# Kernel optimization log

Hardware: AMD Instinct MI355X
Metric: run time of the kernel (lower is better)

Reference implementation:

```python
import jax, jax.numpy as jnp
import numpy as np


def _lstm_dir(x, mask, W, U, b, reverse):
    """Keras-style masked LSTM over one direction.
    x: [B,T,Din], mask: [B,T] bool. Returns (ys [B,T,D], h [B,D], c [B,D]).
    Masked steps: state carried through, emitted output = previous emitted output.
    """
    B, T, _ = x.shape
    D = U.shape[0]
    # Precompute input projections for all timesteps in one big GEMM: [B,T,4D]
    xz = jnp.einsum('btd,dg->btg', x, W) + b
    xz_t = jnp.swapaxes(xz, 0, 1)            # [T,B,4D]
    m_t = jnp.swapaxes(mask, 0, 1)[..., None]  # [T,B,1]
    h0 = jnp.zeros((B, D), x.dtype)

    def step(carry, inp):
        h, c, out_prev = carry
        z_in, m = inp
        z = z_in + h @ U                      # [B,4D]
        i = jax.nn.sigmoid(z[:, :D])
        f = jax.nn.sigmoid(z[:, D:2 * D])
        g = jnp.tanh(z[:, 2 * D:3 * D])
        o = jax.nn.sigmoid(z[:, 3 * D:])
        c_new = f * c + i * g
        h_new = o * jnp.tanh(c_new)
        h = jnp.where(m, h_new, h)
        c = jnp.where(m, c_new, c)
        out = jnp.where(m, h_new, out_prev)
        return (h, c, out), out

    (h, c, _), ys = jax.lax.scan(step, (h0, h0, h0), (xz_t, m_t), reverse=reverse)
    return jnp.swapaxes(ys, 0, 1), h, c


def _bilstm(x, mask, Wf, Uf, bf, Wb, Ub, bb):
    yf, hf, cf = _lstm_dir(x, mask, Wf, Uf, bf, reverse=False)
    yb, hb, cb = _lstm_dir(x, mask, Wb, Ub, bb, reverse=True)
    return jnp.concatenate([yf, yb], axis=-1), hf, cf, hb, cb


def setup_inputs() -> dict:
    key = jax.random.key(0)
    ks = jax.random.split(key, 13)
    B, T, D = 64, 256, 512
    X = jax.random.normal(ks[0], (B, T, D), jnp.float32)
    # variable-length padding: odd batch rows valid for 3T/4 steps, zeros after
    lengths = jnp.where(jnp.arange(B) % 2 == 0, T, 3 * T // 4)
    valid = jnp.arange(T)[None, :] < lengths[:, None]
    X = X * valid[..., None].astype(jnp.float32)
    s = 0.05
    p = lambda k, shp: jax.random.normal(k, shp, jnp.float32) * s
    return {
        'X': X,
        'Wf1': p(ks[1], (D, 4 * D)), 'Uf1': p(ks[2], (D, 4 * D)), 'bf1': jnp.zeros((4 * D,), jnp.float32),
        'Wb1': p(ks[3], (D, 4 * D)), 'Ub1': p(ks[4], (D, 4 * D)), 'bb1': jnp.zeros((4 * D,), jnp.float32),
        'Wf2': p(ks[5], (2 * D, 4 * D)), 'Uf2': p(ks[6], (D, 4 * D)), 'bf2': jnp.zeros((4 * D,), jnp.float32),
        'Wb2': p(ks[7], (2 * D, 4 * D)), 'Ub2': p(ks[8], (D, 4 * D)), 'bb2': jnp.zeros((4 * D,), jnp.float32),
    }


def reference(X, Wf1, Uf1, bf1, Wb1, Ub1, bb1, Wf2, Uf2, bf2, Wb2, Ub2, bb2):
    mask = jnp.any(X != 0, axis=-1)  # Masking(mask_value=0): all-zero timesteps masked
    y1, _, _, _, _ = _bilstm(X, mask, Wf1, Uf1, bf1, Wb1, Ub1, bb1)
    H, h_fw, c_fw, h_bw, c_bw = _bilstm(y1, mask, Wf2, Uf2, bf2, Wb2, Ub2, bb2)
    hidden_state = jnp.concatenate([h_fw, h_bw], axis=-1)
    cell_state = jnp.concatenate([c_fw, c_bw], axis=-1)
    return H, hidden_state, cell_state
```

## Files before the change

### kernel.cpp

```cpp
#include <hip/hip_runtime.h>

typedef unsigned short u16;
typedef unsigned int u32;
typedef unsigned long long u64;
typedef __attribute__((ext_vector_type(8))) short bf16x8;
typedef __attribute__((ext_vector_type(4))) float f32x4;
typedef __attribute__((ext_vector_type(4))) _Float16 f16x4;

#define MFMA16(a, b, c) __builtin_amdgcn_mfma_f32_16x16x32_bf16((a), (b), (c), 0, 0, 0)

__device__ __forceinline__ u16 f2bf(float f) {
    union { float f; u32 u; } v; v.f = f;
    u32 r = v.u + 0x7FFFu + ((v.u >> 16) & 1u);
    return (u16)(r >> 16);
}
__device__ __forceinline__ float sigmoidf_(float x) {
    return 1.0f / (1.0f + __expf(-x));
}
__device__ __forceinline__ float tanhf_(float x) {
    float e = __expf(-2.0f * x);
    return (1.0f - e) / (1.0f + e);
}

__global__ void mask_cast_kernel(const float* __restrict__ X, int* __restrict__ mask,
                                 u16* __restrict__ out) {
    int row = blockIdx.x;
    int lane = threadIdx.x;
    const float* r = X + (size_t)row * 512 + lane * 8;
    float4 v0 = *(const float4*)r;
    float4 v1 = *(const float4*)(r + 4);
    int nz = (v0.x != 0.f) | (v0.y != 0.f) | (v0.z != 0.f) | (v0.w != 0.f) |
             (v1.x != 0.f) | (v1.y != 0.f) | (v1.z != 0.f) | (v1.w != 0.f);
    nz = __any(nz);
    uint4 pk;
    pk.x = (u32)f2bf(v0.x) | ((u32)f2bf(v0.y) << 16);
    pk.y = (u32)f2bf(v0.z) | ((u32)f2bf(v0.w) << 16);
    pk.z = (u32)f2bf(v1.x) | ((u32)f2bf(v1.y) << 16);
    pk.w = (u32)f2bf(v1.z) | ((u32)f2bf(v1.w) << 16);
    *(uint4*)(out + (size_t)row * 512 + lane * 8) = pk;
    if (lane == 0) mask[row] = nz ? 1 : 0;
}

struct TBatch { const float* s[6]; u16* d[6]; };
__global__ void transpose_cast_batch_kernel(TBatch tb, int K, int N) {
    const float* __restrict__ in = tb.s[blockIdx.z];
    u16* __restrict__ out = tb.d[blockIdx.z];
    __shared__ float tile[32][33];
    int k0 = blockIdx.y * 32, n0 = blockIdx.x * 32;
    int tx = threadIdx.x, ty = threadIdx.y;
    #pragma unroll
    for (int i = ty; i < 32; i += 8)
        tile[i][tx] = in[(size_t)(k0 + i) * N + (n0 + tx)];
    __syncthreads();
    #pragma unroll
    for (int i = ty; i < 32; i += 8)
        out[(size_t)(n0 + i) * K + (k0 + tx)] = f2bf(tile[tx][i]);
}

__global__ __launch_bounds__(256) void gemm_xz2_kernel(
        const u16* __restrict__ A,
        const u16* __restrict__ Btf, const u16* __restrict__ Btb,
        const float* __restrict__ biasf, const float* __restrict__ biasb,
        _Float16* __restrict__ Cf, _Float16* __restrict__ Cb, int K) {
    int w = threadIdx.x >> 6, lane = threadIdx.x & 63;
    int q = lane >> 4, col = lane & 15;
    int m0 = blockIdx.x * 256 + w * 64;
    int dir = blockIdx.y >> 4;
    int sl = blockIdx.y & 15;
    const u16* Bt = dir ? Btb : Btf;
    const float* bias = dir ? biasb : biasf;
    _Float16* C = dir ? Cb : Cf;

    const u16* arow = A + (size_t)(m0 + col) * K + q * 8;
    const u16* brow = Bt + (size_t)(sl * 32 + col) * K + q * 8;

    f32x4 acc[4][8];
    #pragma unroll
    for (int mf = 0; mf < 4; ++mf)
        #pragma unroll
        for (int j = 0; j < 8; ++j) acc[mf][j] = (f32x4){0.f, 0.f, 0.f, 0.f};

    #pragma unroll 1
    for (int kc = 0; kc < K; kc += 32) {
        bf16x8 b[8], a[4];
        #pragma unroll
        for (int j = 0; j < 8; ++j) {
            int g = j & 3, half = j >> 2;
            b[j] = *(const bf16x8*)(brow + (size_t)(g * 512 + half * 16) * K + kc);
        }
        #pragma unroll
        for (int mf = 0; mf < 4; ++mf)
            a[mf] = *(const bf16x8*)(arow + (size_t)mf * 16 * K + kc);
        #pragma unroll
        for (int mf = 0; mf < 4; ++mf)
            #pragma unroll
            for (int j = 0; j < 8; ++j)
                acc[mf][j] = MFMA16(a[mf], b[j], acc[mf][j]);
    }

    float bs[8];
    #pragma unroll
    for (int j = 0; j < 8; ++j) {
        int g = j & 3, half = j >> 2;
        bs[j] = bias[g * 512 + sl * 32 + half * 16 + col];
    }

    #pragma unroll
    for (int mf = 0; mf < 4; ++mf) {
        #pragma unroll
        for (int r = 0; r < 4; ++r) {
            int row = m0 + mf * 16 + q * 4 + r;
            int b = row >> 8, t = row & 255;
            #pragma unroll
            for (int half = 0; half < 2; ++half) {
                union { _Float16 h[4]; u64 u; } pk;
                #pragma unroll
                for (int g = 0; g < 4; ++g)
                    pk.h[g] = (_Float16)(acc[mf][half * 4 + g][r] + bs[half * 4 + g]);
                size_t uidx = (((size_t)t * 32 + (sl * 2 + half)) * 64 + b) * 16 + col;
                ((u64*)C)[uidx] = pk.u;
            }
        }
    }
}

__global__ void init_rec_kernel(u32* __restrict__ p, int n) {
    int i = blockIdx.x * 256 + threadIdx.x;
    if (i < n) p[i] = 0;
}

__global__ __launch_bounds__(256) void lstm_rec14_kernel(
        const _Float16* __restrict__ xz_f, const _Float16* __restrict__ xz_b,
        const u16* __restrict__ Ut_f, const u16* __restrict__ Ut_b,
        const int* __restrict__ mask,
        u32* __restrict__ flags,
        u16* __restrict__ hg,
        u16* __restrict__ y_bf,
        float* __restrict__ y_f32,
        float* __restrict__ hc_out)
{
    const int T = 256;
    int slice = blockIdx.x, dir = blockIdx.y;
    int tid = threadIdx.x;
    int lane = tid & 63, q = lane >> 4, col = lane & 15;
    int wv = tid >> 6;
    int ds = slice * 16, m0 = wv * 16;

    const _Float16* xz = dir ? xz_b : xz_f;
    const u16* Ut = dir ? Ut_b : Ut_f;
    u32* planeflags = flags + (dir * 128 + wv * 32) * 16;
    u32* myflag = planeflags + slice * 16;

    alignas(16) __shared__ u16 Ulds[4 * 16 * 64 * 8];
    for (int cell = tid; cell < 4096; cell += 256) {
        int l = cell & 63, fr = cell >> 6;
        int kc = fr & 15, g = fr >> 4;
        *(uint4*)&Ulds[cell * 8] =
            *(const uint4*)(Ut + (size_t)(g * 512 + ds + (l & 15)) * 512 + kc * 32 + (l >> 4) * 8);
    }

    int myrow = m0 + col;
    int cbase = myrow * 4 + (q & 1) * 2 + (q >> 1) * 256;
    int odd = col & 1;
    int r0 = q * 4 + (odd ? 2 : 0);
    size_t pbase = ((size_t)slice * 64 + m0 + r0) * 16 + (col & ~1);

    float creg[4] = {0.f, 0.f, 0.f, 0.f};
    float hreg[4] = {0.f, 0.f, 0.f, 0.f};
    __syncthreads();

    for (int it = 0; it < T; ++it) {
        int t = dir ? (T - 1 - it) : it;
        const u64* hq = (const u64*)(hg + (it & 1) * 65536 + dir * 32768);
        u16* hdst = hg + ((it & 1) ^ 1) * 65536 + dir * 32768;

        f16x4 xzv[4];
        {
            const _Float16* xzt = xz + (((size_t)t * 32 + slice) * 64) * 64;
            #pragma unroll
            for (int r = 0; r < 4; ++r)
                xzv[r] = *(const f16x4*)(xzt + ((m0 + q * 4 + r) * 16 + col) * 4);
        }
        int mk[4];
        #pragma unroll
        for (int r = 0; r < 4; ++r) mk[r] = mask[(m0 + q * 4 + r) * T + t];

        bf16x8 afr[16];
        if (it == 0) {
            #pragma unroll
            for (int c = 0; c < 16; ++c)
                afr[c] = (bf16x8){0, 0, 0, 0, 0, 0, 0, 0};
        } else {
            u32 tgt = (u32)it;
            for (;;) {
                u32 f = __hip_atomic_load(planeflags + (lane & 31) * 16,
                                          __ATOMIC_RELAXED, __HIP_MEMORY_SCOPE_AGENT);
                if (__all(f >= tgt)) break;
                __builtin_amdgcn_s_sleep(1);
            }
            __builtin_amdgcn_sched_barrier(0);
            #pragma unroll
            for (int c = 0; c < 16; ++c) {
                union { u64 qw[2]; bf16x8 v; } u;
                u.qw[0] = __hip_atomic_load(hq + c * 512 + cbase, __ATOMIC_RELAXED,
                                            __HIP_MEMORY_SCOPE_AGENT);
                u.qw[1] = __hip_atomic_load(hq + c * 512 + cbase + 1, __ATOMIC_RELAXED,
                                            __HIP_MEMORY_SCOPE_AGENT);
                afr[c] = u.v;
            }
        }

        f32x4 acc[4];
        #pragma unroll
        for (int g = 0; g < 4; ++g) acc[g] = (f32x4){0.f, 0.f, 0.f, 0.f};
        #pragma unroll
        for (int kc = 0; kc < 16; ++kc) {
            #pragma unroll
            for (int g = 0; g < 4; ++g) {
                bf16x8 b = *(const bf16x8*)&Ulds[((g * 16 + kc) * 64 + lane) * 8];
                acc[g] = MFMA16(afr[kc], b, acc[g]);
            }
        }

        u32 hbv[4];
        #pragma unroll
        for (int r = 0; r < 4; ++r) {
            float zi = acc[0][r] + (float)xzv[r][0];
            float zf = acc[1][r] + (float)xzv[r][1];
            float zg = acc[2][r] + (float)xzv[r][2];
            float zo = acc[3][r] + (float)xzv[r][3];
            float ig = sigmoidf_(zi);
            float fg = sigmoidf_(zf);
            float gg = tanhf_(zg);
            float og = sigmoidf_(zo);
            float cn = fg * creg[r] + ig * gg;
            float hn = og * tanhf_(cn);
            if (mk[r]) { creg[r] = cn; hreg[r] = hn; }
            hbv[r] = (u32)f2bf(hreg[r]);
        }

        if (it < T - 1) {
            u32 part[4];
            #pragma unroll
            for (int r = 0; r < 4; ++r) part[r] = (u32)__shfl_xor((int)hbv[r], 1);
            u32 p0 = odd ? (part[2] | (hbv[2] << 16)) : (hbv[0] | (part[0] << 16));
            u32 p1 = odd ? (part[3] | (hbv[3] << 16)) : (hbv[1] | (part[1] << 16));
            u32* w0 = (u32*)(hdst + pbase);
            u32* w1 = w0 + 8;
            __hip_atomic_store(w0, p0, __ATOMIC_RELAXED, __HIP_MEMORY_SCOPE_AGENT);
            __hip_atomic_store(w1, p1, __ATOMIC_RELAXED, __HIP_MEMORY_SCOPE_AGENT);
            asm volatile("s_waitcnt vmcnt(0)" ::: "memory");
            if (lane == 0)
                __hip_atomic_store(myflag, (u32)(it + 1), __ATOMIC_RELAXED,
                                   __HIP_MEMORY_SCOPE_AGENT);
        }

        #pragma unroll
        for (int r = 0; r < 4; ++r) {
            int b = m0 + q * 4 + r;
            size_t ybase = ((size_t)b * T + t) * 1024 + dir * 512 + ds + col;
            if (y_bf) __builtin_nontemporal_store((u16)hbv[r], y_bf + ybase);
            else      __builtin_nontemporal_store(hreg[r], y_f32 + ybase);
        }
    }

    if (hc_out) {
        #pragma unroll
        for (int r = 0; r < 4; ++r) {
            int b = m0 + q * 4 + r;
            hc_out[(size_t)b * 1024 + dir * 512 + ds + col] = hreg[r];
            hc_out[65536 + (size_t)b * 1024 + dir * 512 + ds + col] = creg[r];
        }
    }
}

extern "C" void kernel_launch(void* const* d_in, const int* in_sizes, int n_in,
                              void* d_out, int out_size, void* d_ws, size_t ws_size,
                              hipStream_t stream) {
    const float* X   = (const float*)d_in[0];
    const float* Wf1 = (const float*)d_in[1];
    const float* Uf1 = (const float*)d_in[2];
    const float* bf1 = (const float*)d_in[3];
    const float* Wb1 = (const float*)d_in[4];
    const float* Ub1 = (const float*)d_in[5];
    const float* bb1 = (const float*)d_in[6];
    const float* Wf2 = (const float*)d_in[7];
    const float* Uf2 = (const float*)d_in[8];
    const float* bf2 = (const float*)d_in[9];
    const float* Wb2 = (const float*)d_in[10];
    const float* Ub2 = (const float*)d_in[11];
    const float* bb2 = (const float*)d_in[12];
    float* out = (float*)d_out;

    u16* y1bf = (u16*)d_out;
    u16* Xbf  = (u16*)((char*)d_out + 33554432);

    char* ws = (char*)d_ws;
    size_t off = 0;
    auto alloc = [&](size_t bytes) { char* p = ws + off; off = (off + bytes + 255) & ~(size_t)255; return p; };
    u16*  Wt1f  = (u16*)alloc(2048ull * 512 * 2);
    u16*  Wt1b  = (u16*)alloc(2048ull * 512 * 2);
    u16*  Wt2f  = (u16*)alloc(2048ull * 1024 * 2);
    u16*  Wt2b  = (u16*)alloc(2048ull * 1024 * 2);
    u16*  Ut1f  = (u16*)alloc(2048ull * 512 * 2);
    u16*  Ut1b  = (u16*)alloc(2048ull * 512 * 2);
    u16*  Ut2f  = (u16*)alloc(2048ull * 512 * 2);
    u16*  Ut2b  = (u16*)alloc(2048ull * 512 * 2);
    int*  maskb = (int*)alloc(16384ull * 4);
    u32*  flags = (u32*)alloc(16384);
    u16*  hg    = (u16*)alloc(2ull * 2 * 32 * 64 * 16 * 2);
    _Float16* xzf = (_Float16*)alloc(16384ull * 2048 * 2);
    _Float16* xzb = (_Float16*)alloc(16384ull * 2048 * 2);
    (void)ws_size; (void)in_sizes; (void)n_in; (void)out_size;
    const int initN = 4096;

    mask_cast_kernel<<<dim3(16384), dim3(64), 0, stream>>>(X, maskb, Xbf);
    TBatch tb6;
    tb6.s[0] = Wf1; tb6.d[0] = Wt1f;
    tb6.s[1] = Wb1; tb6.d[1] = Wt1b;
    tb6.s[2] = Uf1; tb6.d[2] = Ut1f;
    tb6.s[3] = Ub1; tb6.d[3] = Ut1b;
    tb6.s[4] = Uf2; tb6.d[4] = Ut2f;
    tb6.s[5] = Ub2; tb6.d[5] = Ut2b;
    transpose_cast_batch_kernel<<<dim3(64, 16, 6), dim3(32, 8), 0, stream>>>(tb6, 512, 2048);
    TBatch tb2;
    tb2.s[0] = Wf2; tb2.d[0] = Wt2f;
    tb2.s[1] = Wb2; tb2.d[1] = Wt2b;
    tb2.s[2] = nullptr; tb2.d[2] = nullptr;
    tb2.s[3] = nullptr; tb2.d[3] = nullptr;
    tb2.s[4] = nullptr; tb2.d[4] = nullptr;
    tb2.s[5] = nullptr; tb2.d[5] = nullptr;
    transpose_cast_batch_kernel<<<dim3(64, 32, 2), dim3(32, 8), 0, stream>>>(tb2, 1024, 2048);

    gemm_xz2_kernel<<<dim3(64, 32), dim3(256), 0, stream>>>(
        Xbf, Wt1f, Wt1b, bf1, bb1, xzf, xzb, 512);
    init_rec_kernel<<<dim3(16), dim3(256), 0, stream>>>(flags, initN);
    lstm_rec14_kernel<<<dim3(32, 2), dim3(256), 0, stream>>>(
        xzf, xzb, Ut1f, Ut1b, maskb, flags, hg, y1bf, nullptr, nullptr);

    gemm_xz2_kernel<<<dim3(64, 32), dim3(256), 0, stream>>>(
        y1bf, Wt2f, Wt2b, bf2, bb2, xzf, xzb, 1024);
    init_rec_kernel<<<dim3(16), dim3(256), 0, stream>>>(flags, initN);
    lstm_rec14_kernel<<<dim3(32, 2), dim3(256), 0, stream>>>(
        xzf, xzb, Ut2f, Ut2b, maskb, flags, hg, nullptr, out, out + 16777216);
}
```

Before: 2.868 ms.

## Tag hidden-state words with step counter to drop store-wait fence

Hidden-state exchange now packs each 32-bit bf16 pair with the step number in the upper half of a 64-bit atomic store. Readers re-poll the data until every tag matches, so the writer no longer waits on vmcnt(0) before raising its flag. This targets the latency of the per-step cross-block handshake. In exchange the h buffer doubles in size, readers issue twice as many loads, and the init kernel must zero the larger region. The old flag poll is still done before the data poll.

```diff
diff --git a/kernel.cpp b/kernel.cpp
--- a/kernel.cpp
+++ b/kernel.cpp
@@ -129,12 +129,12 @@
     if (i < n) p[i] = 0;
 }
 
-__global__ __launch_bounds__(256) void lstm_rec14_kernel(
+__global__ __launch_bounds__(256) void lstm_rec15_kernel(
         const _Float16* __restrict__ xz_f, const _Float16* __restrict__ xz_b,
         const u16* __restrict__ Ut_f, const u16* __restrict__ Ut_b,
         const int* __restrict__ mask,
         u32* __restrict__ flags,
-        u16* __restrict__ hg,
+        u64* __restrict__ hg,
         u16* __restrict__ y_bf,
         float* __restrict__ y_f32,
         float* __restrict__ hc_out)
@@ -160,10 +160,10 @@
     }
 
     int myrow = m0 + col;
-    int cbase = myrow * 4 + (q & 1) * 2 + (q >> 1) * 256;
+    int cbase = (q >> 1) * 512 + myrow * 8 + (q & 1) * 4;
     int odd = col & 1;
     int r0 = q * 4 + (odd ? 2 : 0);
-    size_t pbase = ((size_t)slice * 64 + m0 + r0) * 16 + (col & ~1);
+    size_t pbase = ((size_t)slice * 64 + m0 + r0) * 8 + (col >> 1);
 
     float creg[4] = {0.f, 0.f, 0.f, 0.f};
     float hreg[4] = {0.f, 0.f, 0.f, 0.f};
@@ -171,8 +171,8 @@
 
     for (int it = 0; it < T; ++it) {
         int t = dir ? (T - 1 - it) : it;
-        const u64* hq = (const u64*)(hg + (it & 1) * 65536 + dir * 32768);
-        u16* hdst = hg + ((it & 1) ^ 1) * 65536 + dir * 32768;
+        const u64* hq = hg + (it & 1) * 32768 + dir * 16384;
+        u64* hdst = hg + ((it & 1) ^ 1) * 32768 + dir * 16384;
 
         f16x4 xzv[4];
         {
@@ -199,14 +199,33 @@
                 __builtin_amdgcn_s_sleep(1);
             }
             __builtin_amdgcn_sched_barrier(0);
-            #pragma unroll
-            for (int c = 0; c < 16; ++c) {
-                union { u64 qw[2]; bf16x8 v; } u;
-                u.qw[0] = __hip_atomic_load(hq + c * 512 + cbase, __ATOMIC_RELAXED,
-                                            __HIP_MEMORY_SCOPE_AGENT);
-                u.qw[1] = __hip_atomic_load(hq + c * 512 + cbase + 1, __ATOMIC_RELAXED,
-                                            __HIP_MEMORY_SCOPE_AGENT);
-                afr[c] = u.v;
+            for (;;) {
+                u64 qv[64];
+                #pragma unroll
+                for (int kc = 0; kc < 16; ++kc) {
+                    #pragma unroll
+                    for (int j = 0; j < 4; ++j)
+                        qv[kc * 4 + j] = __hip_atomic_load(hq + kc * 1024 + cbase + j,
+                                                           __ATOMIC_RELAXED,
+                                                           __HIP_MEMORY_SCOPE_AGENT);
+                }
+                u32 diff = 0;
+                #pragma unroll
+                for (int c = 0; c < 64; ++c)
+                    diff |= ((u32)(qv[c] >> 32)) ^ tgt;
+                if (__builtin_expect(__all(diff == 0), 1)) {
+                    #pragma unroll
+                    for (int kc = 0; kc < 16; ++kc) {
+                        union { u32 w[4]; bf16x8 v; } u;
+                        u.w[0] = (u32)qv[kc * 4 + 0];
+                        u.w[1] = (u32)qv[kc * 4 + 1];
+                        u.w[2] = (u32)qv[kc * 4 + 2];
+                        u.w[3] = (u32)qv[kc * 4 + 3];
+                        afr[kc] = u.v;
+                    }
+                    break;
+                }
+                __builtin_amdgcn_s_sleep(1);
             }
         }
 
@@ -245,11 +264,12 @@
             for (int r = 0; r < 4; ++r) part[r] = (u32)__shfl_xor((int)hbv[r], 1);
             u32 p0 = odd ? (part[2] | (hbv[2] << 16)) : (hbv[0] | (part[0] << 16));
             u32 p1 = odd ? (part[3] | (hbv[3] << 16)) : (hbv[1] | (part[1] << 16));
-            u32* w0 = (u32*)(hdst + pbase);
-            u32* w1 = w0 + 8;
-            __hip_atomic_store(w0, p0, __ATOMIC_RELAXED, __HIP_MEMORY_SCOPE_AGENT);
-            __hip_atomic_store(w1, p1, __ATOMIC_RELAXED, __HIP_MEMORY_SCOPE_AGENT);
-            asm volatile("s_waitcnt vmcnt(0)" ::: "memory");
+            u64 ptag = (u64)(u32)(it + 1) << 32;
+            __hip_atomic_store(hdst + pbase,     (u64)p0 | ptag, __ATOMIC_RELAXED,
+                               __HIP_MEMORY_SCOPE_AGENT);
+            __hip_atomic_store(hdst + pbase + 8, (u64)p1 | ptag, __ATOMIC_RELAXED,
+                               __HIP_MEMORY_SCOPE_AGENT);
+            __builtin_amdgcn_sched_barrier(0);
             if (lane == 0)
                 __hip_atomic_store(myflag, (u32)(it + 1), __ATOMIC_RELAXED,
                                    __HIP_MEMORY_SCOPE_AGENT);
@@ -308,11 +328,11 @@
     u16*  Ut2b  = (u16*)alloc(2048ull * 512 * 2);
     int*  maskb = (int*)alloc(16384ull * 4);
     u32*  flags = (u32*)alloc(16384);
-    u16*  hg    = (u16*)alloc(2ull * 2 * 32 * 64 * 16 * 2);
+    u64*  hg    = (u64*)alloc(2ull * 2 * 32 * 64 * 8 * 8);
     _Float16* xzf = (_Float16*)alloc(16384ull * 2048 * 2);
     _Float16* xzb = (_Float16*)alloc(16384ull * 2048 * 2);
     (void)ws_size; (void)in_sizes; (void)n_in; (void)out_size;
-    const int initN = 4096;
+    const int initN = (16384 + 524288) / 4;
 
     mask_cast_kernel<<<dim3(16384), dim3(64), 0, stream>>>(X, maskb, Xbf);
     TBatch tb6;
@@ -334,13 +354,13 @@
 
     gemm_xz2_kernel<<<dim3(64, 32), dim3(256), 0, stream>>>(
         Xbf, Wt1f, Wt1b, bf1, bb1, xzf, xzb, 512);
-    init_rec_kernel<<<dim3(16), dim3(256), 0, stream>>>(flags, initN);
-    lstm_rec14_kernel<<<dim3(32, 2), dim3(256), 0, stream>>>(
+    init_rec_kernel<<<dim3((initN + 255) / 256), dim3(256), 0, stream>>>(flags, initN);
+    lstm_rec15_kernel<<<dim3(32, 2), dim3(256), 0, stream>>>(
         xzf, xzb, Ut1f, Ut1b, maskb, flags, hg, y1bf, nullptr, nullptr);
 
     gemm_xz2_kernel<<<dim3(64, 32), dim3(256), 0, stream>>>(
         y1bf, Wt2f, Wt2b, bf2, bb2, xzf, xzb, 1024);
-    init_rec_kernel<<<dim3(16), dim3(256), 0, stream>>>(flags, initN);
-    lstm_rec14_kernel<<<dim3(32, 2), dim3(256), 0, stream>>>(
+    init_rec_kernel<<<dim3((initN + 255) / 256), dim3(256), 0, stream>>>(flags, initN);
+    lstm_rec15_kernel<<<dim3(32, 2), dim3(256), 0, stream>>>(
         xzf, xzb, Ut2f, Ut2b, maskb, flags, hg, nullptr, out, out + 16777216);
 }
```

Result: slower. 4.333 ms (+51.1%).
